# Kernel tuning notes

Hardware: AMD Instinct MI355X
Metric: run time of the kernel (lower is better)

The kernel has to match this reference:

```python
import jax, jax.numpy as jnp
import numpy as np

NUM_Q = 1000
B, T = 64, 100
DK, DV, N = 128, 128, 128

def setup_inputs() -> dict:
    key = jax.random.key(0)
    ks = jax.random.split(key, 12)
    return {
        "q": jax.random.randint(ks[0], (B, T), 0, NUM_Q),
        "r": jax.random.randint(ks[1], (B, T), 0, 2),
        "k_emb": jax.random.normal(ks[2], (NUM_Q, DK), jnp.float32) * 0.1,
        "v_emb": jax.random.normal(ks[3], (2 * NUM_Q, DV), jnp.float32) * 0.1,
        "Mk": jax.random.normal(ks[4], (DK, N), jnp.float32) * 0.1,
        "Mv0": jax.random.normal(ks[5], (N, DV), jnp.float32) * 0.1,
        "f_W": jax.random.normal(ks[6], (2 * DK, DK), jnp.float32) * 0.05,
        "f_b": jnp.zeros((DK,), jnp.float32),
        "p_W": jax.random.normal(ks[7], (DK, 1), jnp.float32) * 0.05,
        "p_b": jnp.zeros((1,), jnp.float32),
        "e_W": jax.random.normal(ks[8], (DV, DV), jnp.float32) * 0.05,
        "e_b": jnp.zeros((DV,), jnp.float32),
        "a_W": jax.random.normal(ks[9], (DV, DV), jnp.float32) * 0.05,
        "a_b": jnp.zeros((DV,), jnp.float32),
    }

def reference(q, r, k_emb, v_emb, Mk, Mv0, f_W, f_b, p_W, p_b, e_W, e_b, a_W, a_b):
    num_q = k_emb.shape[0]
    qr = q + num_q * r                                    # [B,T]
    K = k_emb[q].transpose(1, 0, 2)                       # [T,B,DK]
    V = v_emb[qr].transpose(1, 0, 2)                      # [T,B,DV]
    Mvt0 = jnp.broadcast_to(Mv0, (q.shape[0],) + Mv0.shape)  # [B,N,DV]

    def step(Mvt, kv):
        kt, vt = kv                                       # [B,DK],[B,DV]
        wt = jax.nn.softmax(kt @ Mk, axis=-1)             # [B,N] attention weights
        rt = jnp.einsum('bn,bnd->bd', wt, Mvt)            # memory read
        ft = jnp.tanh(jnp.concatenate([rt, kt], axis=-1) @ f_W + f_b)
        pt = jax.nn.sigmoid(ft @ p_W + p_b)               # [B,1]
        et = jax.nn.sigmoid(vt @ e_W + e_b)               # erase gate [B,DV]
        at = jnp.tanh(vt @ a_W + a_b)                     # add vector [B,DV]
        w_ = wt[:, :, None]                               # [B,N,1]
        Mvt = Mvt * (1.0 - w_ * et[:, None, :]) + w_ * at[:, None, :]
        return Mvt, (pt, Mvt)

    _, (p, Mv) = jax.lax.scan(step, Mvt0, (K, V))         # p: [T,B,1], Mv: [T,B,N,DV]
    p = p.reshape(-1, 1)                                  # cat over time, dim=0 -> [T*B,1]
    Mv = Mv.reshape(-1, Mv.shape[-2], Mv.shape[-1])       # [T*B,N,DV]
    return p, Mv
```

## Files before the change

### kernel.cpp

```cpp
#include <hip/hip_runtime.h>
#include <stdint.h>
#include <stddef.h>


constexpr int B = 64;
constexpr int T = 100;
constexpr int D = 128;
constexpr int NUM_Q = 1000;
constexpr int G = 4;
constexpr int CG = 4;
constexpr int BT = B * T;
constexpr int WSTRIDE = BT * D;

typedef float v4f __attribute__((ext_vector_type(4)));

__device__ __forceinline__ float sigmoidf_(float x) {
  return 1.0f / (1.0f + __expf(-x));
}

__global__ __launch_bounds__(128) void kernelA(
    const int* __restrict__ q, const int* __restrict__ r,
    const float* __restrict__ k_emb, const float* __restrict__ v_emb,
    const float* __restrict__ Mk,
    const float* __restrict__ f_W, const float* __restrict__ f_b,
    const float* __restrict__ e_W, const float* __restrict__ e_b,
    const float* __restrict__ a_W, const float* __restrict__ a_b,
    float* __restrict__ ws_w, float* __restrict__ ws_e,
    float* __restrict__ ws_a, float* __restrict__ ws_f)
{
  const int tid = threadIdx.x;
  const int b  = blockIdx.x / (T / G);
  const int tg = blockIdx.x % (T / G);
  const int tbase = tg * G;

  __shared__ float kt[G][D];
  __shared__ float vt[G][D];
  __shared__ float redm[2], reds[2];

  #pragma unroll
  for (int g = 0; g < G; ++g) {
    int idx = b * T + tbase + g;
    int qi  = q[idx];
    int qri = qi + NUM_Q * r[idx];
    kt[g][tid] = k_emb[qi * D + tid];
    vt[g][tid] = v_emb[qri * D + tid];
  }
  __syncthreads();

  float lg[G], se[G], sa[G], sf[G];
  #pragma unroll
  for (int g = 0; g < G; ++g) { lg[g] = 0.f; se[g] = 0.f; sa[g] = 0.f; sf[g] = 0.f; }

  #pragma unroll 4
  for (int k = 0; k < D; ++k) {
    float mk = Mk[k * D + tid];
    float ew = e_W[k * D + tid];
    float aw = a_W[k * D + tid];
    float fw = f_W[(D + k) * D + tid];
    #pragma unroll
    for (int g = 0; g < G; ++g) {
      float kk = kt[g][k];
      float vv = vt[g][k];
      lg[g] = fmaf(kk, mk, lg[g]);
      se[g] = fmaf(vv, ew, se[g]);
      sa[g] = fmaf(vv, aw, sa[g]);
      sf[g] = fmaf(kk, fw, sf[g]);
    }
  }

  const float eb = e_b[tid];
  const float ab = a_b[tid];
  const float fb = f_b[tid];

  for (int g = 0; g < G; ++g) {
    float v = lg[g];
    #pragma unroll
    for (int s = 32; s > 0; s >>= 1) v = fmaxf(v, __shfl_xor(v, s));
    if ((tid & 63) == 0) redm[tid >> 6] = v;
    __syncthreads();
    float mx = fmaxf(redm[0], redm[1]);
    float ex = __expf(lg[g] - mx);
    v = ex;
    #pragma unroll
    for (int s = 32; s > 0; s >>= 1) v += __shfl_xor(v, s);
    if ((tid & 63) == 0) reds[tid >> 6] = v;
    __syncthreads();
    float sm = reds[0] + reds[1];

    int idx = (b * T + tbase + g) * D + tid;
    ws_w[idx] = ex / sm;
    ws_e[idx] = sigmoidf_(se[g] + eb);
    ws_a[idx] = tanhf(sa[g] + ab);
    ws_f[idx] = sf[g] + fb;
  }
}

__global__ __launch_bounds__(256) void kernelB(
    const float* __restrict__ Mv0,
    const float* __restrict__ ws_w, const float* __restrict__ ws_e,
    const float* __restrict__ ws_a,
    float* __restrict__ out_Mv, float* __restrict__ ws_rt)
{
  const int b  = blockIdx.x >> 3;
  const int nt = blockIdx.x & 7;
  const int tid = threadIdx.x;
  const int nrow = tid >> 4;
  const int dgrp = tid & 15;
  const int n  = nt * 16 + nrow;
  const int d0 = dgrp * 8;
  const int wave = tid >> 6;
  const int lane = tid & 63;

  __shared__ float part[2][4][16][8];

  float m[8];
  #pragma unroll
  for (int i = 0; i < 8; ++i) m[i] = Mv0[n * D + d0 + i];

  const float*  pw = ws_w + (size_t)(b * T) * D + n;
  const float4* pe = (const float4*)(ws_e + (size_t)(b * T) * D + d0);
  const float4* pa = (const float4*)(ws_a + (size_t)(b * T) * D + d0);

  float  wv = pw[0];
  float4 e0 = pe[0], e1 = pe[1], a0 = pa[0], a1 = pa[1];

  for (int t = 0; t < T; ++t) {
    const int tn = (t + 1 < T) ? (t + 1) : t;
    float  wn  = pw[(size_t)tn * D];
    float4 en0 = pe[(size_t)tn * 32], en1 = pe[(size_t)tn * 32 + 1];
    float4 an0 = pa[(size_t)tn * 32], an1 = pa[(size_t)tn * 32 + 1];

    float pr[8];
    #pragma unroll
    for (int i = 0; i < 8; ++i) pr[i] = wv * m[i];
    #pragma unroll
    for (int i = 0; i < 8; ++i) {
      pr[i] += __shfl_xor(pr[i], 16);
      pr[i] += __shfl_xor(pr[i], 32);
    }
    if (lane < 16) {
      #pragma unroll
      for (int i = 0; i < 8; ++i) part[t & 1][wave][lane][i] = pr[i];
    }

    float ee[8] = {e0.x, e0.y, e0.z, e0.w, e1.x, e1.y, e1.z, e1.w};
    float aa[8] = {a0.x, a0.y, a0.z, a0.w, a1.x, a1.y, a1.z, a1.w};
    #pragma unroll
    for (int i = 0; i < 8; ++i) {
      m[i] = m[i] * (1.0f - wv * ee[i]) + wv * aa[i];
    }

    size_t obase = ((size_t)(t * B + b) * D + n) * D + d0;
    v4f o0 = {m[0], m[1], m[2], m[3]};
    v4f o1 = {m[4], m[5], m[6], m[7]};
    __builtin_nontemporal_store(o0, (v4f*)(out_Mv + obase));
    __builtin_nontemporal_store(o1, (v4f*)(out_Mv + obase + 4));

    __syncthreads();
    if (tid < D) {
      const int dg = tid >> 3, di = tid & 7;
      float s = part[t & 1][0][dg][di] + part[t & 1][1][dg][di]
              + part[t & 1][2][dg][di] + part[t & 1][3][dg][di];
      ws_rt[((size_t)(b * T + t) * 8 + nt) * D + tid] = s;
    }

    wv = wn; e0 = en0; e1 = en1; a0 = an0; a1 = an1;
  }
}

__global__ __launch_bounds__(128) void kernelC(
    const float* __restrict__ f_W,
    const float* __restrict__ p_W,
    const float* __restrict__ p_b,
    const float* __restrict__ ws_f, const float* __restrict__ ws_rt,
    float* __restrict__ out_p)
{
  const int grp = blockIdx.x;
  const int b  = grp / (T / CG);
  const int tg = grp % (T / CG);
  const int t0 = tg * CG;
  const int bt0 = b * T + t0;
  const int tid = threadIdx.x;

  __shared__ float rsh[CG][D];
  __shared__ float wred[CG][2];

  float fa[CG];
  #pragma unroll
  for (int g = 0; g < CG; ++g) {
    const float* prt = ws_rt + (size_t)(bt0 + g) * (8 * D);
    float rt = 0.f;
    #pragma unroll
    for (int nt = 0; nt < 8; ++nt) rt += prt[nt * D + tid];
    rsh[g][tid] = rt;
    fa[g] = ws_f[(bt0 + g) * D + tid];
  }
  __syncthreads();

  #pragma unroll 4
  for (int d2 = 0; d2 < D; ++d2) {
    float fw = f_W[d2 * D + tid];
    #pragma unroll
    for (int g = 0; g < CG; ++g) fa[g] = fmaf(rsh[g][d2], fw, fa[g]);
  }

  const float pw = p_W[tid];
  #pragma unroll
  for (int g = 0; g < CG; ++g) {
    float v = tanhf(fa[g]) * pw;
    #pragma unroll
    for (int s = 32; s > 0; s >>= 1) v += __shfl_xor(v, s);
    if ((tid & 63) == 0) wred[g][tid >> 6] = v;
  }
  __syncthreads();
  if (tid < CG) {
    float pt = sigmoidf_(wred[tid][0] + wred[tid][1] + p_b[0]);
    out_p[(t0 + tid) * B + b] = pt;
  }
}

extern "C" void kernel_launch(void* const* d_in, const int* in_sizes, int n_in,
                              void* d_out, int out_size, void* d_ws, size_t ws_size,
                              hipStream_t stream)
{
  const int* q = (const int*)d_in[0];
  const int* r = (const int*)d_in[1];
  const float* k_emb = (const float*)d_in[2];
  const float* v_emb = (const float*)d_in[3];
  const float* Mk   = (const float*)d_in[4];
  const float* Mv0  = (const float*)d_in[5];
  const float* f_W  = (const float*)d_in[6];
  const float* f_b  = (const float*)d_in[7];
  const float* p_W  = (const float*)d_in[8];
  const float* p_b  = (const float*)d_in[9];
  const float* e_W  = (const float*)d_in[10];
  const float* e_b  = (const float*)d_in[11];
  const float* a_W  = (const float*)d_in[12];
  const float* a_b  = (const float*)d_in[13];

  float* ws   = (float*)d_ws;
  float* ws_w = ws;
  float* ws_e = ws + (size_t)WSTRIDE;
  float* ws_a = ws + (size_t)2 * WSTRIDE;
  float* ws_f = ws + (size_t)3 * WSTRIDE;
  float* ws_rt = ws + (size_t)4 * WSTRIDE;

  float* out    = (float*)d_out;
  float* out_p  = out;
  float* out_Mv = out + BT;

  hipLaunchKernelGGL(kernelA, dim3(B * (T / G)), dim3(D), 0, stream,
                     q, r, k_emb, v_emb, Mk, f_W, f_b, e_W, e_b, a_W, a_b,
                     ws_w, ws_e, ws_a, ws_f);
  hipLaunchKernelGGL(kernelB, dim3(B * 8), dim3(256), 0, stream,
                     Mv0, ws_w, ws_e, ws_a, out_Mv, ws_rt);
  hipLaunchKernelGGL(kernelC, dim3(B * (T / CG)), dim3(D), 0, stream,
                     f_W, p_W, p_b, ws_f, ws_rt, out_p);
}
```

Before: 589.3 us.

## Split memory recurrence into 16 N-tiles per batch with XCD-aware block mapping

The recurrence kernel now uses 16 blocks per batch instead of 8, each covering 8 memory rows with 4 columns per thread. This doubles the grid to 1024 blocks so more CUs share the sequential time loop and the large Mv output write. Block indices are also permuted so consecutive blocks land on different batches, which is meant to spread work across chiplets. In exchange, the partial-read workspace and the downstream reduction in kernelC double to 16 tiles, and each thread does less work per synchronisation.

```diff
diff --git a/kernel.cpp b/kernel.cpp
--- a/kernel.cpp
+++ b/kernel.cpp
@@ -11,6 +11,7 @@
 constexpr int CG = 4;
 constexpr int BT = B * T;
 constexpr int WSTRIDE = BT * D;
+constexpr int NTILES = 16;
 
 typedef float v4f __attribute__((ext_vector_type(4)));
 
@@ -101,70 +102,68 @@
     const float* __restrict__ ws_a,
     float* __restrict__ out_Mv, float* __restrict__ ws_rt)
 {
-  const int b  = blockIdx.x >> 3;
-  const int nt = blockIdx.x & 7;
+  const int j = blockIdx.x;
+  const int b  = ((j & 7) << 3) | ((j >> 3) & 7);
+  const int nt = j >> 6;
   const int tid = threadIdx.x;
-  const int nrow = tid >> 4;
-  const int dgrp = tid & 15;
-  const int n  = nt * 16 + nrow;
-  const int d0 = dgrp * 8;
+  const int nrow = tid >> 5;
+  const int dgrp = tid & 31;
+  const int n  = nt * 8 + nrow;
+  const int d0 = dgrp * 4;
   const int wave = tid >> 6;
   const int lane = tid & 63;
 
-  __shared__ float part[2][4][16][8];
-
-  float m[8];
-  #pragma unroll
-  for (int i = 0; i < 8; ++i) m[i] = Mv0[n * D + d0 + i];
+  __shared__ float part[2][4][32][4];
+
+  float m[4];
+  #pragma unroll
+  for (int i = 0; i < 4; ++i) m[i] = Mv0[n * D + d0 + i];
 
   const float*  pw = ws_w + (size_t)(b * T) * D + n;
   const float4* pe = (const float4*)(ws_e + (size_t)(b * T) * D + d0);
   const float4* pa = (const float4*)(ws_a + (size_t)(b * T) * D + d0);
 
   float  wv = pw[0];
-  float4 e0 = pe[0], e1 = pe[1], a0 = pa[0], a1 = pa[1];
+  float4 ev = pe[0];
+  float4 av = pa[0];
 
   for (int t = 0; t < T; ++t) {
     const int tn = (t + 1 < T) ? (t + 1) : t;
-    float  wn  = pw[(size_t)tn * D];
-    float4 en0 = pe[(size_t)tn * 32], en1 = pe[(size_t)tn * 32 + 1];
-    float4 an0 = pa[(size_t)tn * 32], an1 = pa[(size_t)tn * 32 + 1];
-
-    float pr[8];
-    #pragma unroll
-    for (int i = 0; i < 8; ++i) pr[i] = wv * m[i];
-    #pragma unroll
-    for (int i = 0; i < 8; ++i) {
-      pr[i] += __shfl_xor(pr[i], 16);
-      pr[i] += __shfl_xor(pr[i], 32);
-    }
-    if (lane < 16) {
-      #pragma unroll
-      for (int i = 0; i < 8; ++i) part[t & 1][wave][lane][i] = pr[i];
-    }
-
-    float ee[8] = {e0.x, e0.y, e0.z, e0.w, e1.x, e1.y, e1.z, e1.w};
-    float aa[8] = {a0.x, a0.y, a0.z, a0.w, a1.x, a1.y, a1.z, a1.w};
-    #pragma unroll
-    for (int i = 0; i < 8; ++i) {
+    float  wn = pw[(size_t)tn * D];
+    float4 en = pe[(size_t)tn * 32];
+    float4 an = pa[(size_t)tn * 32];
+
+    float prx = wv * m[0], pry = wv * m[1], prz = wv * m[2], prw = wv * m[3];
+    prx += __shfl_xor(prx, 32);
+    pry += __shfl_xor(pry, 32);
+    prz += __shfl_xor(prz, 32);
+    prw += __shfl_xor(prw, 32);
+    if (lane < 32) {
+      float4 pr4 = make_float4(prx, pry, prz, prw);
+      *(float4*)&part[t & 1][wave][dgrp][0] = pr4;
+    }
+
+    float ee[4] = {ev.x, ev.y, ev.z, ev.w};
+    float aa[4] = {av.x, av.y, av.z, av.w};
+    #pragma unroll
+    for (int i = 0; i < 4; ++i) {
       m[i] = m[i] * (1.0f - wv * ee[i]) + wv * aa[i];
     }
 
     size_t obase = ((size_t)(t * B + b) * D + n) * D + d0;
     v4f o0 = {m[0], m[1], m[2], m[3]};
-    v4f o1 = {m[4], m[5], m[6], m[7]};
     __builtin_nontemporal_store(o0, (v4f*)(out_Mv + obase));
-    __builtin_nontemporal_store(o1, (v4f*)(out_Mv + obase + 4));
 
     __syncthreads();
     if (tid < D) {
-      const int dg = tid >> 3, di = tid & 7;
-      float s = part[t & 1][0][dg][di] + part[t & 1][1][dg][di]
-              + part[t & 1][2][dg][di] + part[t & 1][3][dg][di];
-      ws_rt[((size_t)(b * T + t) * 8 + nt) * D + tid] = s;
-    }
-
-    wv = wn; e0 = en0; e1 = en1; a0 = an0; a1 = an1;
+      float s = part[t & 1][0][tid >> 2][tid & 3]
+              + part[t & 1][1][tid >> 2][tid & 3]
+              + part[t & 1][2][tid >> 2][tid & 3]
+              + part[t & 1][3][tid >> 2][tid & 3];
+      ws_rt[((size_t)(b * T + t) * NTILES + nt) * D + tid] = s;
+    }
+
+    wv = wn; ev = en; av = an;
   }
 }
 
@@ -188,10 +187,10 @@
   float fa[CG];
   #pragma unroll
   for (int g = 0; g < CG; ++g) {
-    const float* prt = ws_rt + (size_t)(bt0 + g) * (8 * D);
+    const float* prt = ws_rt + (size_t)(bt0 + g) * (NTILES * D);
     float rt = 0.f;
     #pragma unroll
-    for (int nt = 0; nt < 8; ++nt) rt += prt[nt * D + tid];
+    for (int nt = 0; nt < NTILES; ++nt) rt += prt[nt * D + tid];
     rsh[g][tid] = rt;
     fa[g] = ws_f[(bt0 + g) * D + tid];
   }
@@ -252,7 +251,7 @@
   hipLaunchKernelGGL(kernelA, dim3(B * (T / G)), dim3(D), 0, stream,
                      q, r, k_emb, v_emb, Mk, f_W, f_b, e_W, e_b, a_W, a_b,
                      ws_w, ws_e, ws_a, ws_f);
-  hipLaunchKernelGGL(kernelB, dim3(B * 8), dim3(256), 0, stream,
+  hipLaunchKernelGGL(kernelB, dim3(B * NTILES), dim3(256), 0, stream,
                      Mv0, ws_w, ws_e, ws_a, out_Mv, ws_rt);
   hipLaunchKernelGGL(kernelC, dim3(B * (T / CG)), dim3(D), 0, stream,
                      f_W, p_W, p_b, ws_f, ws_rt, out_p);
```

New measurement: 504.3 us. -14.4%, faster.
